# Kernel tuning notes

Hardware: AMD Instinct MI355X
Metric: run time of the kernel (lower is better)

The kernel has to match this reference:

```python
import jax, jax.numpy as jnp
import numpy as np

N_NODES = 50000


def gcn_conv(x, W, b, row, col, edge_weight):
    # PyG GCNConv (add_self_loops=False, normalize=True):
    # 1) linear transform, 2) symmetric normalization, 3) scatter-add aggregation
    h = x @ W  # [N, F_out]
    deg = jax.ops.segment_sum(edge_weight, col, num_segments=N_NODES)  # [N]
    dinv = jnp.where(deg > 0, jax.lax.rsqrt(deg), 0.0)
    norm = dinv[row] * edge_weight * dinv[col]  # [E]
    msgs = norm[:, None] * h[row]  # [E, F_out] gather
    out = jax.ops.segment_sum(msgs, col, num_segments=N_NODES)  # scatter-add
    return out + b


def setup_inputs() -> dict:
    key = jax.random.key(0)
    ks = jax.random.split(key, 7)
    E = 800000
    IN, HID, OUT = 256, 128, 16
    x = jax.random.normal(ks[0], (N_NODES, IN), dtype=jnp.float32)
    edge_index = jax.random.randint(ks[1], (2, E), 0, N_NODES, dtype=jnp.int64)
    edge_weight = jax.random.uniform(ks[2], (E,), dtype=jnp.float32)
    W1 = jax.random.normal(ks[3], (IN, HID), dtype=jnp.float32) * (1.0 / np.sqrt(IN))
    b1 = jnp.zeros((HID,), dtype=jnp.float32)
    W2 = jax.random.normal(ks[4], (HID, OUT), dtype=jnp.float32) * (1.0 / np.sqrt(HID))
    b2 = jnp.zeros((OUT,), dtype=jnp.float32)
    return {"x": x, "edge_index": edge_index, "edge_weight": edge_weight,
            "W1": W1, "b1": b1, "W2": W2, "b2": b2}


def reference(x, edge_index, edge_weight, W1, b1, W2, b2):
    row, col = edge_index[0], edge_index[1]
    h = jax.nn.relu(gcn_conv(x, W1, b1, row, col, edge_weight))
    # dropout is identity in eval mode
    h = gcn_conv(h, W2, b2, row, col, edge_weight)
    return jax.nn.log_softmax(h, axis=1)
```

## Files before the change

kernel.cpp:

```cpp
#include <hip/hip_runtime.h>
#include <hip/hip_bf16.h>

#define NN 50000
#define EE 800000
#define FIN 256
#define FH 128
#define FO 16
#define MAXDEG 64

using short8 = __attribute__((ext_vector_type(8))) short;
using f32x4  = __attribute__((ext_vector_type(4))) float;

__device__ __forceinline__ unsigned short f2b(float f) {
    unsigned int u = __float_as_uint(f);
    u += 0x7fffu + ((u >> 16) & 1u);
    return (unsigned short)(u >> 16);
}
__device__ __forceinline__ float b2f(unsigned short h) {
    return __uint_as_float(((unsigned int)h) << 16);
}

__global__ void detect_k(const unsigned int* __restrict__ ei, int* __restrict__ flag) {
    int t = threadIdx.x;
    unsigned int v = (t < 32) ? ei[2 * t + 1] : 0u;
    unsigned long long ball = __ballot(v != 0u);
    if (t == 0) *flag = (ball == 0ull) ? 1 : 0;
}

__global__ void zero_k(int* __restrict__ cursor) {
    int i = blockIdx.x * 256 + threadIdx.x;
    if (i < NN) cursor[i] = 0;
}

__device__ __forceinline__ void decode_edge(const void* ei, int int64flag, int e,
                                            int& r, int& c) {
    if (int64flag) {
        const long long* p = (const long long*)ei;
        r = (int)p[e]; c = (int)p[EE + e];
    } else {
        const int* p = (const int*)ei;
        r = p[e]; c = p[EE + e];
    }
    r = min(max(r, 0), NN - 1);
    c = min(max(c, 0), NN - 1);
}

__global__ void scatterpad_k(const void* __restrict__ ei, const float* __restrict__ ew,
                             const int* __restrict__ flag, int* __restrict__ cursor,
                             unsigned int* __restrict__ padj) {
    int e = blockIdx.x * 256 + threadIdx.x;
    if (e >= EE) return;
    int r, c;
    decode_edge(ei, *flag, e, r, c);
    float w = ew[e];
    int pos = atomicAdd(&cursor[c], 1);
    if (pos < MAXDEG)
        padj[c * MAXDEG + pos] = ((unsigned int)r << 16) | (unsigned int)f2b(w);
}

__global__ __launch_bounds__(256) void deg_k(const int* __restrict__ cursor,
                                             const unsigned int* __restrict__ padj,
                                             float* __restrict__ dinv) {
    const int n = blockIdx.x * 16 + (threadIdx.x >> 4);
    const int f = threadIdx.x & 15;
    const int cnt = min(cursor[n], MAXDEG);
    const unsigned int* base = padj + n * MAXDEG;
    float s = 0.f;
    for (int j = f; j < cnt; j += 16) s += b2f((unsigned short)(base[j] & 0xffff));
#pragma unroll
    for (int d = 1; d < 16; d <<= 1) s += __shfl_xor(s, d);
    if (f == 0) dinv[n] = (s > 0.f) ? rsqrtf(s) : 0.f;
}

__global__ void cvt_w_k(const float* __restrict__ W1, const float* __restrict__ W2,
                        unsigned short* __restrict__ w1t, unsigned short* __restrict__ w2t) {
    int i = blockIdx.x * 256 + threadIdx.x;
    if (i < FH * FIN) {
        int n = i / FIN, k = i % FIN;
        w1t[i] = f2b(W1[k * FH + n]);
    }
    int j = i - FH * FIN;
    if (j >= 0 && j < FO * FH) {
        int n = j / FH, k = j % FH;
        w2t[j] = f2b(W2[k * FO + n]);
    }
}

__global__ __launch_bounds__(256) void gemm1_k(const float* __restrict__ X,
                                               const unsigned short* __restrict__ Bt,
                                               const float* __restrict__ dinv,
                                               unsigned short* __restrict__ C) {
    const int lane = threadIdx.x & 63;
    const int wave = threadIdx.x >> 6;
    const int m0 = blockIdx.x * 128 + wave * 32;
    const int lr = lane & 15;
    const int lk = (lane >> 4) * 8;
    f32x4 acc[2][8];
#pragma unroll
    for (int i = 0; i < 2; i++)
#pragma unroll
        for (int j = 0; j < 8; j++) acc[i][j] = (f32x4){0.f, 0.f, 0.f, 0.f};

    for (int k0 = 0; k0 < FIN; k0 += 32) {
        short8 a[2], b[8];
#pragma unroll
        for (int mi = 0; mi < 2; mi++) {
            int row = m0 + mi * 16 + lr;
            if (row >= NN) row = NN - 1;
            const float* ap = X + (size_t)row * FIN + k0 + lk;
            float4 v0 = *(const float4*)ap;
            float4 v1 = *(const float4*)(ap + 4);
            a[mi][0] = (short)f2b(v0.x); a[mi][1] = (short)f2b(v0.y);
            a[mi][2] = (short)f2b(v0.z); a[mi][3] = (short)f2b(v0.w);
            a[mi][4] = (short)f2b(v1.x); a[mi][5] = (short)f2b(v1.y);
            a[mi][6] = (short)f2b(v1.z); a[mi][7] = (short)f2b(v1.w);
        }
#pragma unroll
        for (int ni = 0; ni < 8; ni++)
            b[ni] = *(const short8*)(Bt + (ni * 16 + lr) * FIN + k0 + lk);
#pragma unroll
        for (int mi = 0; mi < 2; mi++)
#pragma unroll
            for (int ni = 0; ni < 8; ni++)
                acc[mi][ni] = __builtin_amdgcn_mfma_f32_16x16x32_bf16(
                    a[mi], b[ni], acc[mi][ni], 0, 0, 0);
    }
    const int r0 = (lane >> 4) * 4;
#pragma unroll
    for (int mi = 0; mi < 2; mi++)
#pragma unroll
        for (int r = 0; r < 4; r++) {
            int row = m0 + mi * 16 + r0 + r;
            if (row < NN) {
                float dv = dinv[row];
#pragma unroll
                for (int ni = 0; ni < 8; ni++)
                    C[(size_t)row * FH + ni * 16 + lr] = f2b(acc[mi][ni][r] * dv);
            }
        }
}

__global__ __launch_bounds__(256) void gemm2_k(const unsigned short* __restrict__ A,
                                               const unsigned short* __restrict__ Bt,
                                               const float* __restrict__ dinv,
                                               unsigned short* __restrict__ C) {
    const int lane = threadIdx.x & 63;
    const int wave = threadIdx.x >> 6;
    const int m0 = blockIdx.x * 128 + wave * 32;
    const int lr = lane & 15;
    const int lk = (lane >> 4) * 8;
    f32x4 acc[2];
    acc[0] = (f32x4){0.f, 0.f, 0.f, 0.f};
    acc[1] = (f32x4){0.f, 0.f, 0.f, 0.f};

    for (int k0 = 0; k0 < FH; k0 += 32) {
        short8 a[2], b;
#pragma unroll
        for (int mi = 0; mi < 2; mi++) {
            int row = m0 + mi * 16 + lr;
            if (row >= NN) row = NN - 1;
            a[mi] = *(const short8*)(A + (size_t)row * FH + k0 + lk);
        }
        b = *(const short8*)(Bt + lr * FH + k0 + lk);
#pragma unroll
        for (int mi = 0; mi < 2; mi++)
            acc[mi] = __builtin_amdgcn_mfma_f32_16x16x32_bf16(a[mi], b, acc[mi], 0, 0, 0);
    }
    const int r0 = (lane >> 4) * 4;
#pragma unroll
    for (int mi = 0; mi < 2; mi++)
#pragma unroll
        for (int r = 0; r < 4; r++) {
            int row = m0 + mi * 16 + r0 + r;
            if (row < NN) {
                float dv = dinv[row];
                C[(size_t)row * FO + lr] = f2b(acc[mi][r] * dv);
            }
        }
}

__global__ __launch_bounds__(256) void agg1_k(const int* __restrict__ cursor,
                                              const unsigned int* __restrict__ padj,
                                              const unsigned short* __restrict__ hlin,
                                              const float* __restrict__ dinv,
                                              const float* __restrict__ bias1,
                                              unsigned short* __restrict__ h1) {
    const int wid = blockIdx.x * 4 + (threadIdx.x >> 6);
    const int lane = threadIdx.x & 63;
    const int cnt = min(__builtin_amdgcn_readfirstlane(cursor[wid]), MAXDEG);
    const unsigned int* base = padj + wid * MAXDEG;
    const unsigned short* hp = hlin + 2 * lane;

    float a0 = 0.f, a1 = 0.f, b0 = 0.f, b1v = 0.f;
    float c0 = 0.f, c1 = 0.f, d0 = 0.f, d1 = 0.f;
    int j = 0;
    for (; j + 4 <= cnt; j += 4) {
        unsigned int u0 = base[j + 0], u1 = base[j + 1];
        unsigned int u2 = base[j + 2], u3 = base[j + 3];
        unsigned int g0 = *(const unsigned int*)(hp + (size_t)(u0 >> 16) * FH);
        unsigned int g1 = *(const unsigned int*)(hp + (size_t)(u1 >> 16) * FH);
        unsigned int g2 = *(const unsigned int*)(hp + (size_t)(u2 >> 16) * FH);
        unsigned int g3 = *(const unsigned int*)(hp + (size_t)(u3 >> 16) * FH);
        float n0 = b2f((unsigned short)(u0 & 0xffff));
        float n1 = b2f((unsigned short)(u1 & 0xffff));
        float n2 = b2f((unsigned short)(u2 & 0xffff));
        float n3 = b2f((unsigned short)(u3 & 0xffff));
        a0  += n0 * b2f((unsigned short)(g0 & 0xffff));
        a1  += n0 * b2f((unsigned short)(g0 >> 16));
        b0  += n1 * b2f((unsigned short)(g1 & 0xffff));
        b1v += n1 * b2f((unsigned short)(g1 >> 16));
        c0  += n2 * b2f((unsigned short)(g2 & 0xffff));
        c1  += n2 * b2f((unsigned short)(g2 >> 16));
        d0  += n3 * b2f((unsigned short)(g3 & 0xffff));
        d1  += n3 * b2f((unsigned short)(g3 >> 16));
    }
    for (; j < cnt; j++) {
        unsigned int u = base[j];
        unsigned int g = *(const unsigned int*)(hp + (size_t)(u >> 16) * FH);
        float n = b2f((unsigned short)(u & 0xffff));
        a0 += n * b2f((unsigned short)(g & 0xffff));
        a1 += n * b2f((unsigned short)(g >> 16));
    }
    float dc = dinv[wid];
    float r0 = dc * ((a0 + b0) + (c0 + d0)) + bias1[2 * lane];
    float r1 = dc * ((a1 + b1v) + (c1 + d1)) + bias1[2 * lane + 1];
    unsigned int w = (unsigned int)f2b(fmaxf(r0, 0.f)) |
                     ((unsigned int)f2b(fmaxf(r1, 0.f)) << 16);
    *(unsigned int*)(h1 + (size_t)wid * FH + 2 * lane) = w;
}

__global__ __launch_bounds__(256) void agg2_k(const int* __restrict__ cursor,
                                              const unsigned int* __restrict__ padj,
                                              const unsigned short* __restrict__ h2lin,
                                              const float* __restrict__ dinv,
                                              const float* __restrict__ bias2,
                                              float* __restrict__ out) {
    const int g = threadIdx.x >> 4, f = threadIdx.x & 15;
    const int n = blockIdx.x * 16 + g;
    const int cnt = min(cursor[n], MAXDEG);
    const unsigned int* base = padj + n * MAXDEG;
    float a0 = 0.f, a1 = 0.f, a2 = 0.f, a3 = 0.f;
    int j = 0;
    for (; j + 4 <= cnt; j += 4) {
        unsigned int u0 = base[j + 0], u1 = base[j + 1];
        unsigned int u2 = base[j + 2], u3 = base[j + 3];
        float v0 = b2f(h2lin[(size_t)(u0 >> 16) * FO + f]);
        float v1 = b2f(h2lin[(size_t)(u1 >> 16) * FO + f]);
        float v2 = b2f(h2lin[(size_t)(u2 >> 16) * FO + f]);
        float v3 = b2f(h2lin[(size_t)(u3 >> 16) * FO + f]);
        a0 += b2f((unsigned short)(u0 & 0xffff)) * v0;
        a1 += b2f((unsigned short)(u1 & 0xffff)) * v1;
        a2 += b2f((unsigned short)(u2 & 0xffff)) * v2;
        a3 += b2f((unsigned short)(u3 & 0xffff)) * v3;
    }
    for (; j < cnt; j++) {
        unsigned int u = base[j];
        a0 += b2f((unsigned short)(u & 0xffff)) * b2f(h2lin[(size_t)(u >> 16) * FO + f]);
    }
    float acc = dinv[n] * (((a0 + a1) + (a2 + a3))) + bias2[f];
    float m = acc;
#pragma unroll
    for (int d = 1; d < 16; d <<= 1) m = fmaxf(m, __shfl_xor(m, d));
    float ex = expf(acc - m);
    float sum = ex;
#pragma unroll
    for (int d = 1; d < 16; d <<= 1) sum += __shfl_xor(sum, d);
    out[(size_t)n * FO + f] = acc - m - logf(sum);
}

extern "C" void kernel_launch(void* const* d_in, const int* in_sizes, int n_in,
                              void* d_out, int out_size, void* d_ws, size_t ws_size,
                              hipStream_t stream) {
    const float* x  = (const float*)d_in[0];
    const void*  ei = d_in[1];
    const float* ew = (const float*)d_in[2];
    const float* W1 = (const float*)d_in[3];
    const float* b1 = (const float*)d_in[4];
    const float* W2 = (const float*)d_in[5];
    const float* b2 = (const float*)d_in[6];
    float* out = (float*)d_out;

    char* base = (char*)d_ws;
    size_t off = 0;
    auto alloc = [&](size_t bytes) {
        void* p = base + off;
        off += (bytes + 255) & ~(size_t)255;
        return p;
    };
    int*          flag   = (int*)alloc(4);
    int*          cursor = (int*)alloc(NN * 4);
    float*        dinv   = (float*)alloc(NN * 4);
    unsigned int* padj   = (unsigned int*)alloc((size_t)NN * MAXDEG * 4);
    unsigned short* w1t   = (unsigned short*)alloc(FH * FIN * 2);
    unsigned short* w2t   = (unsigned short*)alloc(FO * FH * 2);
    unsigned short* h1lin = (unsigned short*)alloc((size_t)NN * FH * 2);
    unsigned short* h1    = (unsigned short*)alloc((size_t)NN * FH * 2);
    unsigned short* h2lin = (unsigned short*)alloc((size_t)NN * FO * 2);
    (void)ws_size; (void)n_in; (void)in_sizes; (void)out_size;

    const int NB = (NN + 255) / 256;

    detect_k<<<1, 64, 0, stream>>>((const unsigned int*)ei, flag);
    zero_k<<<NB, 256, 0, stream>>>(cursor);
    scatterpad_k<<<EE / 256, 256, 0, stream>>>(ei, ew, flag, cursor, padj);
    deg_k<<<NN / 16, 256, 0, stream>>>(cursor, padj, dinv);

    cvt_w_k<<<(FH * FIN + FO * FH + 255) / 256, 256, 0, stream>>>(W1, W2, w1t, w2t);

    gemm1_k<<<(NN + 127) / 128, 256, 0, stream>>>(x, w1t, dinv, h1lin);
    agg1_k<<<NN / 4, 256, 0, stream>>>(cursor, padj, h1lin, dinv, b1, h1);
    gemm2_k<<<(NN + 127) / 128, 256, 0, stream>>>(h1, w2t, dinv, h2lin);
    agg2_k<<<NN / 16, 256, 0, stream>>>(cursor, padj, h2lin, dinv, b2, out);
}
```

Baseline: 228.3 us.

## Fuse prep kernels, co-schedule edge scatter with GEMM1, fold normalization into edge weights

Merges the detect, zero and weight-convert kernels into one prep kernel. Runs the edge scatter and the first GEMM in a single launch split by block index, which is possible once GEMM1 no longer depends on dinv. Folds dinv[row]*w*dinv[col] into the padded adjacency weights through a new rewrite pass, so the aggregation and GEMM2 kernels skip their dinv scaling. This costs an extra pass over the adjacency and rounds the combined normalized weight to bf16 once, where before each factor was applied separately.

```diff
diff --git a/kernel.cpp b/kernel.cpp
--- a/kernel.cpp
+++ b/kernel.cpp
@@ -7,6 +7,8 @@
 #define FH 128
 #define FO 16
 #define MAXDEG 64
+#define SCB (EE / 256)
+#define G1B ((NN + 127) / 128)
 
 using short8 = __attribute__((ext_vector_type(8))) short;
 using f32x4  = __attribute__((ext_vector_type(4))) float;
@@ -20,16 +22,25 @@
     return __uint_as_float(((unsigned int)h) << 16);
 }
 
-__global__ void detect_k(const unsigned int* __restrict__ ei, int* __restrict__ flag) {
-    int t = threadIdx.x;
-    unsigned int v = (t < 32) ? ei[2 * t + 1] : 0u;
-    unsigned long long ball = __ballot(v != 0u);
-    if (t == 0) *flag = (ball == 0ull) ? 1 : 0;
-}
-
-__global__ void zero_k(int* __restrict__ cursor) {
+__global__ void prep_k(const unsigned int* __restrict__ ei, int* __restrict__ flag,
+                       int* __restrict__ cursor,
+                       const float* __restrict__ W1, const float* __restrict__ W2,
+                       unsigned short* __restrict__ w1t, unsigned short* __restrict__ w2t) {
     int i = blockIdx.x * 256 + threadIdx.x;
+    if (blockIdx.x == 0 && threadIdx.x < 64) {
+        unsigned int v = (threadIdx.x < 32) ? ei[2 * threadIdx.x + 1] : 0u;
+        unsigned long long ball = __ballot(v != 0u);
+        if (threadIdx.x == 0) *flag = (ball == 0ull) ? 1 : 0;
+    }
     if (i < NN) cursor[i] = 0;
+    if (i < FH * FIN) {
+        int n = i / FIN, k = i % FIN;
+        w1t[i] = f2b(W1[k * FH + n]);
+    }
+    if (i < FO * FH) {
+        int n = i / FH, k = i % FH;
+        w2t[i] = f2b(W2[k * FO + n]);
+    }
 }
 
 __device__ __forceinline__ void decode_edge(const void* ei, int int64flag, int e,
@@ -45,54 +56,28 @@
     c = min(max(c, 0), NN - 1);
 }
 
-__global__ void scatterpad_k(const void* __restrict__ ei, const float* __restrict__ ew,
-                             const int* __restrict__ flag, int* __restrict__ cursor,
-                             unsigned int* __restrict__ padj) {
-    int e = blockIdx.x * 256 + threadIdx.x;
-    if (e >= EE) return;
-    int r, c;
-    decode_edge(ei, *flag, e, r, c);
-    float w = ew[e];
-    int pos = atomicAdd(&cursor[c], 1);
-    if (pos < MAXDEG)
-        padj[c * MAXDEG + pos] = ((unsigned int)r << 16) | (unsigned int)f2b(w);
-}
-
-__global__ __launch_bounds__(256) void deg_k(const int* __restrict__ cursor,
-                                             const unsigned int* __restrict__ padj,
-                                             float* __restrict__ dinv) {
-    const int n = blockIdx.x * 16 + (threadIdx.x >> 4);
-    const int f = threadIdx.x & 15;
-    const int cnt = min(cursor[n], MAXDEG);
-    const unsigned int* base = padj + n * MAXDEG;
-    float s = 0.f;
-    for (int j = f; j < cnt; j += 16) s += b2f((unsigned short)(base[j] & 0xffff));
-#pragma unroll
-    for (int d = 1; d < 16; d <<= 1) s += __shfl_xor(s, d);
-    if (f == 0) dinv[n] = (s > 0.f) ? rsqrtf(s) : 0.f;
-}
-
-__global__ void cvt_w_k(const float* __restrict__ W1, const float* __restrict__ W2,
-                        unsigned short* __restrict__ w1t, unsigned short* __restrict__ w2t) {
-    int i = blockIdx.x * 256 + threadIdx.x;
-    if (i < FH * FIN) {
-        int n = i / FIN, k = i % FIN;
-        w1t[i] = f2b(W1[k * FH + n]);
-    }
-    int j = i - FH * FIN;
-    if (j >= 0 && j < FO * FH) {
-        int n = j / FH, k = j % FH;
-        w2t[j] = f2b(W2[k * FO + n]);
-    }
-}
-
-__global__ __launch_bounds__(256) void gemm1_k(const float* __restrict__ X,
+__global__ __launch_bounds__(256) void fused_k(const void* __restrict__ ei,
+                                               const float* __restrict__ ew,
+                                               const int* __restrict__ flag,
+                                               int* __restrict__ cursor,
+                                               unsigned int* __restrict__ padj,
+                                               const float* __restrict__ X,
                                                const unsigned short* __restrict__ Bt,
-                                               const float* __restrict__ dinv,
                                                unsigned short* __restrict__ C) {
+    if (blockIdx.x < SCB) {
+        int e = blockIdx.x * 256 + threadIdx.x;
+        int r, c;
+        decode_edge(ei, *flag, e, r, c);
+        float w = ew[e];
+        int pos = atomicAdd(&cursor[c], 1);
+        if (pos < MAXDEG)
+            padj[c * MAXDEG + pos] = ((unsigned int)r << 16) | (unsigned int)f2b(w);
+        return;
+    }
+    const int bx = blockIdx.x - SCB;
     const int lane = threadIdx.x & 63;
     const int wave = threadIdx.x >> 6;
-    const int m0 = blockIdx.x * 128 + wave * 32;
+    const int m0 = bx * 128 + wave * 32;
     const int lr = lane & 15;
     const int lk = (lane >> 4) * 8;
     f32x4 acc[2][8];
@@ -132,57 +117,44 @@
         for (int r = 0; r < 4; r++) {
             int row = m0 + mi * 16 + r0 + r;
             if (row < NN) {
-                float dv = dinv[row];
 #pragma unroll
                 for (int ni = 0; ni < 8; ni++)
-                    C[(size_t)row * FH + ni * 16 + lr] = f2b(acc[mi][ni][r] * dv);
+                    C[(size_t)row * FH + ni * 16 + lr] = f2b(acc[mi][ni][r]);
             }
         }
 }
 
-__global__ __launch_bounds__(256) void gemm2_k(const unsigned short* __restrict__ A,
-                                               const unsigned short* __restrict__ Bt,
-                                               const float* __restrict__ dinv,
-                                               unsigned short* __restrict__ C) {
-    const int lane = threadIdx.x & 63;
-    const int wave = threadIdx.x >> 6;
-    const int m0 = blockIdx.x * 128 + wave * 32;
-    const int lr = lane & 15;
-    const int lk = (lane >> 4) * 8;
-    f32x4 acc[2];
-    acc[0] = (f32x4){0.f, 0.f, 0.f, 0.f};
-    acc[1] = (f32x4){0.f, 0.f, 0.f, 0.f};
-
-    for (int k0 = 0; k0 < FH; k0 += 32) {
-        short8 a[2], b;
-#pragma unroll
-        for (int mi = 0; mi < 2; mi++) {
-            int row = m0 + mi * 16 + lr;
-            if (row >= NN) row = NN - 1;
-            a[mi] = *(const short8*)(A + (size_t)row * FH + k0 + lk);
-        }
-        b = *(const short8*)(Bt + lr * FH + k0 + lk);
-#pragma unroll
-        for (int mi = 0; mi < 2; mi++)
-            acc[mi] = __builtin_amdgcn_mfma_f32_16x16x32_bf16(a[mi], b, acc[mi], 0, 0, 0);
-    }
-    const int r0 = (lane >> 4) * 4;
-#pragma unroll
-    for (int mi = 0; mi < 2; mi++)
-#pragma unroll
-        for (int r = 0; r < 4; r++) {
-            int row = m0 + mi * 16 + r0 + r;
-            if (row < NN) {
-                float dv = dinv[row];
-                C[(size_t)row * FO + lr] = f2b(acc[mi][r] * dv);
-            }
-        }
+__global__ __launch_bounds__(256) void deg_k(const int* __restrict__ cursor,
+                                             const unsigned int* __restrict__ padj,
+                                             float* __restrict__ dinv) {
+    const int n = blockIdx.x * 16 + (threadIdx.x >> 4);
+    const int f = threadIdx.x & 15;
+    const int cnt = min(cursor[n], MAXDEG);
+    const unsigned int* base = padj + n * MAXDEG;
+    float s = 0.f;
+    for (int j = f; j < cnt; j += 16) s += b2f((unsigned short)(base[j] & 0xffff));
+#pragma unroll
+    for (int d = 1; d < 16; d <<= 1) s += __shfl_xor(s, d);
+    if (f == 0) dinv[n] = (s > 0.f) ? rsqrtf(s) : 0.f;
+}
+
+__global__ void rewrite_k(const int* __restrict__ cursor, const float* __restrict__ dinv,
+                          unsigned int* __restrict__ padj) {
+    int i = blockIdx.x * 256 + threadIdx.x;
+    int n = i >> 6, j = i & 63;
+    if (n >= NN) return;
+    if (j < min(cursor[n], MAXDEG)) {
+        unsigned int u = padj[i];
+        int r = u >> 16;
+        float w = b2f((unsigned short)(u & 0xffff));
+        float nw = dinv[n] * w * dinv[r];
+        padj[i] = (u & 0xffff0000u) | (unsigned int)f2b(nw);
+    }
 }
 
 __global__ __launch_bounds__(256) void agg1_k(const int* __restrict__ cursor,
                                               const unsigned int* __restrict__ padj,
                                               const unsigned short* __restrict__ hlin,
-                                              const float* __restrict__ dinv,
                                               const float* __restrict__ bias1,
                                               unsigned short* __restrict__ h1) {
     const int wid = blockIdx.x * 4 + (threadIdx.x >> 6);
@@ -221,18 +193,51 @@
         a0 += n * b2f((unsigned short)(g & 0xffff));
         a1 += n * b2f((unsigned short)(g >> 16));
     }
-    float dc = dinv[wid];
-    float r0 = dc * ((a0 + b0) + (c0 + d0)) + bias1[2 * lane];
-    float r1 = dc * ((a1 + b1v) + (c1 + d1)) + bias1[2 * lane + 1];
+    float r0 = ((a0 + b0) + (c0 + d0)) + bias1[2 * lane];
+    float r1 = ((a1 + b1v) + (c1 + d1)) + bias1[2 * lane + 1];
     unsigned int w = (unsigned int)f2b(fmaxf(r0, 0.f)) |
                      ((unsigned int)f2b(fmaxf(r1, 0.f)) << 16);
     *(unsigned int*)(h1 + (size_t)wid * FH + 2 * lane) = w;
 }
 
+__global__ __launch_bounds__(256) void gemm2_k(const unsigned short* __restrict__ A,
+                                               const unsigned short* __restrict__ Bt,
+                                               unsigned short* __restrict__ C) {
+    const int lane = threadIdx.x & 63;
+    const int wave = threadIdx.x >> 6;
+    const int m0 = blockIdx.x * 128 + wave * 32;
+    const int lr = lane & 15;
+    const int lk = (lane >> 4) * 8;
+    f32x4 acc[2];
+    acc[0] = (f32x4){0.f, 0.f, 0.f, 0.f};
+    acc[1] = (f32x4){0.f, 0.f, 0.f, 0.f};
+
+    for (int k0 = 0; k0 < FH; k0 += 32) {
+        short8 a[2], b;
+#pragma unroll
+        for (int mi = 0; mi < 2; mi++) {
+            int row = m0 + mi * 16 + lr;
+            if (row >= NN) row = NN - 1;
+            a[mi] = *(const short8*)(A + (size_t)row * FH + k0 + lk);
+        }
+        b = *(const short8*)(Bt + lr * FH + k0 + lk);
+#pragma unroll
+        for (int mi = 0; mi < 2; mi++)
+            acc[mi] = __builtin_amdgcn_mfma_f32_16x16x32_bf16(a[mi], b, acc[mi], 0, 0, 0);
+    }
+    const int r0 = (lane >> 4) * 4;
+#pragma unroll
+    for (int mi = 0; mi < 2; mi++)
+#pragma unroll
+        for (int r = 0; r < 4; r++) {
+            int row = m0 + mi * 16 + r0 + r;
+            if (row < NN) C[(size_t)row * FO + lr] = f2b(acc[mi][r]);
+        }
+}
+
 __global__ __launch_bounds__(256) void agg2_k(const int* __restrict__ cursor,
                                               const unsigned int* __restrict__ padj,
                                               const unsigned short* __restrict__ h2lin,
-                                              const float* __restrict__ dinv,
                                               const float* __restrict__ bias2,
                                               float* __restrict__ out) {
     const int g = threadIdx.x >> 4, f = threadIdx.x & 15;
@@ -257,7 +262,7 @@
         unsigned int u = base[j];
         a0 += b2f((unsigned short)(u & 0xffff)) * b2f(h2lin[(size_t)(u >> 16) * FO + f]);
     }
-    float acc = dinv[n] * (((a0 + a1) + (a2 + a3))) + bias2[f];
+    float acc = ((a0 + a1) + (a2 + a3)) + bias2[f];
     float m = acc;
 #pragma unroll
     for (int d = 1; d < 16; d <<= 1) m = fmaxf(m, __shfl_xor(m, d));
@@ -300,15 +305,11 @@
 
     const int NB = (NN + 255) / 256;
 
-    detect_k<<<1, 64, 0, stream>>>((const unsigned int*)ei, flag);
-    zero_k<<<NB, 256, 0, stream>>>(cursor);
-    scatterpad_k<<<EE / 256, 256, 0, stream>>>(ei, ew, flag, cursor, padj);
+    prep_k<<<NB, 256, 0, stream>>>((const unsigned int*)ei, flag, cursor, W1, W2, w1t, w2t);
+    fused_k<<<SCB + G1B, 256, 0, stream>>>(ei, ew, flag, cursor, padj, x, w1t, h1lin);
     deg_k<<<NN / 16, 256, 0, stream>>>(cursor, padj, dinv);
-
-    cvt_w_k<<<(FH * FIN + FO * FH + 255) / 256, 256, 0, stream>>>(W1, W2, w1t, w2t);
-
-    gemm1_k<<<(NN + 127) / 128, 256, 0, stream>>>(x, w1t, dinv, h1lin);
-    agg1_k<<<NN / 4, 256, 0, stream>>>(cursor, padj, h1lin, dinv, b1, h1);
-    gemm2_k<<<(NN + 127) / 128, 256, 0, stream>>>(h1, w2t, dinv, h2lin);
-    agg2_k<<<NN / 16, 256, 0, stream>>>(cursor, padj, h2lin, dinv, b2, out);
-}
+    rewrite_k<<<NN * MAXDEG / 256, 256, 0, stream>>>(cursor, dinv, padj);
+    agg1_k<<<NN / 4, 256, 0, stream>>>(cursor, padj, h1lin, b1, h1);
+    gemm2_k<<<(NN + 127) / 128, 256, 0, stream>>>(h1, w2t, h2lin);
+    agg2_k<<<NN / 16, 256, 0, stream>>>(cursor, padj, h2lin, b2, out);
+}
```

After: 231.8 us. No clear change (+1.6%).
